# Kernel tuning notes

Measured on AMD Instinct MI355X. Metric: run time of the kernel, lower is better.

## Reference

```python
import jax, jax.numpy as jnp
import numpy as np

J, L, A, A_PRIME, C_CH = 4, 4, 2, 2, 1
B, M, N = 4, 128, 128


def _compute_idx():
    # mirrors CorrLayerDownsample.compute_idx with delta_j=J, delta_l=L,
    # shift_mode='samec' and num_channels=1 (to_shift_color always True)
    dj, dl = J, L
    la1, la2, shifted = [], [], []
    for c1 in range(C_CH):
        for c2 in range(C_CH):
            for j1 in range(J):
                for j2 in range(j1, min(j1 + 1 + dj, J)):
                    for l1 in range(L):
                        for l2 in range(max(0, l1 + 1 - dl), min(L, l1 + 1 + dl)):
                            for a1 in range(A):
                                for a2 in range(A_PRIME):
                                    la1.append((j1, A * L * c1 + A * l1 + a1))
                                    la2.append((j2, A * L * c2 + A * l2 + a2))
                                    shifted.append(j2 + 1)
    return (np.asarray(la1, np.int32), np.asarray(la2, np.int32),
            np.asarray(shifted, np.int32))


def _make_masks():
    # stand-in for create_masks_shift: mask 0 = zero shift only; mask k (k>=1)
    # = wrapped square neighborhood of radius 2**(k-1) (shift scale grows with j2)
    xs = np.minimum(np.arange(M), M - np.arange(M))
    ys = np.minimum(np.arange(N), N - np.arange(N))
    masks = np.zeros((J + 1, M, N), np.float32)
    masks[0, 0, 0] = 1.0
    for k in range(1, J + 1):
        r = 2 ** (k - 1)
        masks[k] = ((xs[:, None] <= r) & (ys[None, :] <= r)).astype(np.float32)
    return masks


def setup_inputs() -> dict:
    key = jax.random.key(0)
    la1, la2, shifted = _compute_idx()
    masks = _make_masks()
    union_idx = np.where(masks.sum(0).reshape(-1) > 0)[0].astype(np.int32)
    xpsi = jax.random.normal(key, (J, B, C_CH * L * A, M, N), dtype=jnp.float32)
    return {
        "xpsi": xpsi,
        "masks_shift": jnp.asarray(masks),
        "la1": jnp.asarray(la1),
        "la2": jnp.asarray(la2),
        "shifted": jnp.asarray(shifted),
        "union_idx": jnp.asarray(union_idx),
    }


def reference(xpsi, masks_shift, la1, la2, shifted, union_idx):
    # xpsi: [J, B, C, M, N] real. FFT once per (scale, channel) map.
    hatx = jnp.fft.fft2(xpsi)                     # [J, B, C, M, N] complex64
    # gather the (scale, la-channel) pair for every moment (all scales same size,
    # so the per-(j1,j2) loop + upsample of the original collapses to one gather)
    h1 = hatx[la1[:, 0], :, la1[:, 1]]            # [P, B, M, N]
    h2 = hatx[la2[:, 0], :, la2[:, 1]]            # [P, B, M, N]
    corr = jnp.fft.ifft2(h1 * jnp.conj(h2)).real  # [P, B, M, N]
    masked = corr * masks_shift[shifted][:, None]  # per-moment shift mask
    P, Bb, Mm, Nn = masked.shape
    # flatten=True path: keep only positions in the union of all shift masks
    return masked.reshape(P, Bb, Mm * Nn)[:, :, union_idx]
```

## Files before the change

### kernel.cpp

```cpp
#include <hip/hip_runtime.h>

typedef __attribute__((ext_vector_type(8))) short short8;
typedef __attribute__((ext_vector_type(4))) float float4v;
typedef __attribute__((address_space(1))) const unsigned int gu32;
typedef __attribute__((address_space(3))) unsigned int lu32;

#define TPB 256
#define NXPSI (4*4*8*16384)
#define NGR   (NXPSI/4)
#define ZPG   64
#define PBYTE (NXPSI*2 + ZPG*8)
#define NPART 3207168
#define NOUT  739840

__device__ __constant__ int TBASE[19] = {
    0, 278528, 557056, 835584, 1114112, 1392640, 1671168, 1949696, 2228224,
    2506752, 2617344, 2727936, 2838528, 2949120,
    3059712, 3100672, 3141632,
    3182592, 3194880};

static __device__ __forceinline__ unsigned short f2bf(float f) {
    unsigned int u = __builtin_bit_cast(unsigned int, f);
    u = (u + 0x7FFFu + ((u >> 16) & 1u)) >> 16;
    return (unsigned short)u;
}

__global__ __launch_bounds__(256)
void conv_bf16(const float* __restrict__ in, unsigned short* __restrict__ outw) {
    const int g = blockIdx.x * 256 + threadIdx.x;
    if (g < NGR) {
        const float4 v = reinterpret_cast<const float4*>(in)[g];
        reinterpret_cast<ushort4*>(outw)[g] =
            ushort4{f2bf(v.x), f2bf(v.y), f2bf(v.z), f2bf(v.w)};
    } else if (g < NGR + ZPG) {
        reinterpret_cast<ushort4*>(outw)[g] = ushort4{0, 0, 0, 0};
    }
}

template<int J2, bool PRE, bool PART>
static __device__ __forceinline__ void corr_body(
        const float* __restrict__ xpsi, const unsigned short* __restrict__ xbf,
        float* __restrict__ out, float* __restrict__ part,
        unsigned char* smem, int tgl, int n0, int moff, int b, int kc)
{
    constexpr int R    = 1 << J2;
    constexpr int DXN  = 2 * R + 1;
    constexpr int DYN  = DXN;
    constexpr int MV   = 8 * (J2 + 1);
    constexpr int ROWS = 16 + 2 * R;
    constexpr int ABUF = 16 * 256;
    constexpr int S    = DYN * MV * 16;
    constexpr int W    = (J2 == 0) ? 8 : 16;

    unsigned short* a_lds = (unsigned short*)smem;
    unsigned short* b_lds = (unsigned short*)(smem + 4 * ABUF);

    const int k0    = kc * 16;
    const int vrows = (MV - moff < 16) ? MV - moff : 16;

    const int ch2lo = n0 / DXN;
    int nhi = n0 + W - 1; if (nhi > 8 * DXN - 1) nhi = 8 * DXN - 1;
    const int nimg = nhi / DXN - ch2lo + 1;

    const int tid  = threadIdx.x;
    const int lane = tid & 63;
    const int wv   = tid >> 6;
    const int c    = lane & 15;
    const int g    = lane >> 4;

    const int ncol    = n0 + c;
    const bool validn = (ncol < 8 * DXN) && (J2 > 0 || c < 8);
    const int ncc     = validn ? ncol : n0;
    const int ch2     = ncc / DXN;
    const int dxi     = ncc - ch2 * DXN;
    const int dx      = dxi - R;
    const int xo      = dx < 0 ? dx + 17 : dx;
    const int bst     = ((ch2 - ch2lo) * ROWS + (2 * R - dxi)) * 152;

    auto stageA = [&](int sub, int bufi) {
        unsigned short* ab = a_lds + bufi * ABUF;
        #pragma unroll
        for (int it = 0; it < 2; ++it) {
            const int o  = it * TPB + tid;
            const int ms = o >> 5;
            const int lo = (o & 31) ^ ms;
            const int me = moff + ms;
            const int j1 = me >> 3, ch1 = me & 7;
            if (PRE) {
                const unsigned short* src = (ms < vrows)
                    ? xbf + ((((size_t)j1*4 + b)*8) + ch1) * 16384
                          + (k0 + sub * 2 + (lo >> 4)) * 128 + ((lo & 15) << 3)
                    : xbf + NXPSI + ((lo & 31) << 3);
                __builtin_amdgcn_global_load_lds((gu32*)src, (lu32*)(ab + o * 8), 16, 0, 0);
            } else {
                ushort4 w0{0,0,0,0}, w1{0,0,0,0};
                if (ms < vrows) {
                    const float* s = xpsi + ((((size_t)j1*4 + b)*8) + ch1) * 16384
                                   + (k0 + sub * 2 + (lo >> 4)) * 128 + ((lo & 15) << 3);
                    const float4 f0 = ((const float4*)s)[0];
                    const float4 f1 = ((const float4*)s)[1];
                    w0 = ushort4{f2bf(f0.x), f2bf(f0.y), f2bf(f0.z), f2bf(f0.w)};
                    w1 = ushort4{f2bf(f1.x), f2bf(f1.y), f2bf(f1.z), f2bf(f1.w)};
                }
                *(ushort4*)(ab + o * 8)     = w0;
                *(ushort4*)(ab + o * 8 + 4) = w1;
            }
        }
    };

    stageA(0, 0);

    if (PRE && J2 >= 2) {
        for (int ci = 0; ci < nimg; ++ci) {
            const unsigned short* img = xbf + ((((size_t)J2*4 + b)*8) + ch2lo + ci) * 16384;
            const int ng2 = ROWS * 36;
            for (int i = tid; i < ng2; i += TPB) {
                const int tr = i / 36, tc = (i - tr * 36) * 4;
                const int sr = (k0 - R + tr) & 127;
                const int sc = (tc + R - 16) & 127;
                *(ushort4*)(b_lds + (ci * ROWS + tr) * 152 + tc) =
                    *(const ushort4*)(img + sr * 128 + sc);
            }
        }
    } else {
        const int tot = nimg * ROWS * 144;
        for (int i = tid; i < tot; i += TPB) {
            const int ci = i / (ROWS * 144);
            const int rr = i - ci * (ROWS * 144);
            const int tr = rr / 144, tc = rr - tr * 144;
            const int sr = (k0 - R + tr) & 127;
            const int sc = (tc + R - 16) & 127;
            b_lds[(ci * ROWS + tr) * 152 + tc] = PRE
                ? xbf[((((size_t)J2*4 + b)*8) + ch2lo + ci) * 16384 + sr * 128 + sc]
                : f2bf(xpsi[((((size_t)J2*4 + b)*8) + ch2lo + ci) * 16384 + sr * 128 + sc]);
        }
    }

    float4v acc[DYN];
    #pragma unroll
    for (int i = 0; i < DYN; ++i) acc[i] = (float4v)0.f;

    auto compute = [&](int sub, int bufi) {
        const char* abase = (const char*)(a_lds + bufi * ABUF);
        #pragma unroll
        for (int i2 = 0; i2 < 2; ++i2) {
            const int loff = (((i2 << 8) | (wv << 6) | (g << 4))) ^ (c << 4);
            const short8 af0 = *(const short8*)(abase + c * 512 + loff);

            const unsigned short* bp = b_lds + bst + (sub * 2 + i2) * 152
                                     + (wv << 5) + (g << 3);
            const uint4 wA = *(const uint4*)bp;
            const uint4 wB = *(const uint4*)(bp + 8);
            const uint4 wC = *(const uint4*)(bp + 16);
            const unsigned int wd[12] = {wA.x,wA.y,wA.z,wA.w, wB.x,wB.y,wB.z,wB.w,
                                         wC.x,wC.y,wC.z,wC.w};
            __builtin_amdgcn_s_setprio(1);
            #pragma unroll
            for (int dyi = 0; dyi < DYN; ++dyi) {
                unsigned int o0, o1, o2, o3;
                if ((dyi & 1) == 0) {
                    const int bb = 8 - (dyi >> 1);
                    o0 = wd[bb]; o1 = wd[bb+1]; o2 = wd[bb+2]; o3 = wd[bb+3];
                } else {
                    const int bb = (15 - dyi) >> 1;
                    o0 = (wd[bb]   >> 16) | (wd[bb+1] << 16);
                    o1 = (wd[bb+1] >> 16) | (wd[bb+2] << 16);
                    o2 = (wd[bb+2] >> 16) | (wd[bb+3] << 16);
                    o3 = (wd[bb+3] >> 16) | (wd[bb+4] << 16);
                }
                union { unsigned int u[4]; short8 s; } bq;
                bq.u[0] = o0; bq.u[1] = o1; bq.u[2] = o2; bq.u[3] = o3;
                acc[dyi] = __builtin_amdgcn_mfma_f32_16x16x32_bf16(
                    af0, bq.s, acc[dyi], 0, 0, 0);
            }
            __builtin_amdgcn_s_setprio(0);
        }
    };

    __syncthreads();
    for (int sub = 0; sub < 8; ++sub) {
        if (sub < 7) stageA(sub + 1, (sub + 1) & 1);
        compute(sub, sub & 1);
        __syncthreads();
    }

    if (PART) {
        constexpr int NG  = (DYN < 9) ? DYN : 9;
        constexpr int NPH = (DYN + NG - 1) / NG;
        float* red = (float*)smem;
        float* pt  = part + TBASE[tgl] + (size_t)(kc * 4 + b) * S;
        const int cpart0 = n0 & 15;
        #pragma unroll
        for (int ph = 0; ph < NPH; ++ph) {
            const int d0 = ph * NG;
            const int nd = (DYN - d0 < NG) ? (DYN - d0) : NG;
            __syncthreads();
            #pragma unroll
            for (int dl = 0; dl < NG; ++dl) {
                if (dl >= nd) break;
                *(float4v*)(red + ((wv * NG + dl) * 64 + lane) * 4) = acc[d0 + dl];
            }
            __syncthreads();
            for (int i = tid; i < nd * 64; i += TPB) {
                const int dl = i >> 6;
                const int ln = i & 63;
                const float4v s0 = *(const float4v*)(red + ((0 * NG + dl) * 64 + ln) * 4);
                const float4v s1 = *(const float4v*)(red + ((1 * NG + dl) * 64 + ln) * 4);
                const float4v s2 = *(const float4v*)(red + ((2 * NG + dl) * 64 + ln) * 4);
                const float4v s3 = *(const float4v*)(red + ((3 * NG + dl) * 64 + ln) * 4);
                const float4v s = (s0 + s1) + (s2 + s3);
                const int cc = ln & 15, gg = ln >> 4;
                if ((n0 + cc < 8 * DXN) && (J2 > 0 || cc < 8)) {
                    const int dyi = d0 + dl;
                    #pragma unroll
                    for (int t2 = 0; t2 < 4; ++t2) {
                        const int ml = (gg << 2) + t2;
                        if (ml < vrows)
                            pt[(dyi * MV + moff + ml) * 16 + cpart0 + cc] = s[t2];
                    }
                }
            }
        }
        return;
    }

    if (!validn) return;
    #pragma unroll
    for (int dyi = 0; dyi < DYN; ++dyi) {
        const int dy = dyi - R;
        const int yo = dy < 0 ? dy + 17 : dy;
        #pragma unroll
        for (int t2 = 0; t2 < 4; ++t2) {
            const int ml = (g << 2) + t2;
            if (ml >= vrows) continue;
            const int m = moff + ml;
            const int j1 = m >> 3, ch1 = m & 7;
            const int pb = ((j1 * (9 - j1)) >> 1) + (J2 - j1);
            const int p  = pb * 64 + ((ch1 >> 1) << 4) + ((ch2 >> 1) << 2)
                         + ((ch1 & 1) << 1) + (ch2 & 1);
            atomicAdd(out + (size_t)(p * 4 + b) * 289 + xo * 17 + yo, acc[dyi][t2]);
        }
    }
}

template<bool PRE, bool PART>
__global__ __launch_bounds__(TPB, 3)
void corr_v8(const float* __restrict__ xpsi, const unsigned short* __restrict__ xbf,
             float* __restrict__ out, float* __restrict__ part)
{
    __shared__ __align__(16) unsigned char smem[40704];
    const int bid = blockIdx.x;
    const int g8  = bid & 7;
    const int b   = g8 >> 1;
    const int mh  = g8 & 1;
    const int w   = bid >> 3;
    const int kc  = w / 17;
    const int s   = w - kc * 17;
    if (s < 9)
        corr_body<3, PRE, PART>(xpsi, xbf, out, part, smem, s, 16 * s, 16 * mh, b, kc);
    else if (s < 14)
        corr_body<2, PRE, PART>(xpsi, xbf, out, part, smem, s, 16 * (s - 9), 16 * mh, b, kc);
    else if (mh == 0)
        corr_body<1, PRE, PART>(xpsi, xbf, out, part, smem, s, 16 * (s - 14), 0, b, kc);
    else
        corr_body<0, PRE, PART>(xpsi, xbf, out, part, smem,
                                (s < 16) ? 17 : 18, 8 * (s - 14), 0, b, kc);
}

__global__ __launch_bounds__(256)
void reduce2(const float* __restrict__ part, float* __restrict__ out)
{
    const int t  = blockIdx.y;
    const int j2 = (t < 9) ? 3 : (t < 14) ? 2 : (t < 17) ? 1 : 0;
    const int nt = t - ((t < 9) ? 0 : (t < 14) ? 9 : (t < 17) ? 14 : 17);
    const int R = 1 << j2, DXN = 2 * R + 1, DYN = DXN, MV = 8 * (j2 + 1);
    const int S = DYN * MV * 16;
    const int tot = 4 * DYN * MV * 4;
    const int i = blockIdx.x * 256 + threadIdx.x;
    if (i >= tot) return;
    const int c4 = (i & 3) << 2;
    int r2 = i >> 2;
    const int m = r2 % MV;  r2 /= MV;
    const int dyi = r2 % DYN;
    const int b   = r2 / DYN;
    const int ncol0 = nt * 16 + c4;
    if (ncol0 >= 8 * DXN) return;
    const float* q = part + TBASE[t] + (size_t)b * S + (dyi * MV + m) * 16 + c4;
    float4 v = {0.f, 0.f, 0.f, 0.f};
    #pragma unroll
    for (int qq = 0; qq < 8; ++qq) {
        const float4 w = *(const float4*)(q + (size_t)qq * 4 * S);
        v.x += w.x; v.y += w.y; v.z += w.z; v.w += w.w;
    }
    const int dy = dyi - R;
    const int yo = dy < 0 ? dy + 17 : dy;
    const int j1 = m >> 3, ch1 = m & 7;
    const int pb = ((j1 * (9 - j1)) >> 1) + (j2 - j1);
    const float vv[4] = {v.x, v.y, v.z, v.w};
    #pragma unroll
    for (int e = 0; e < 4; ++e) {
        const int ncol = ncol0 + e;
        if (ncol >= 8 * DXN) break;
        const int ch2 = ncol / DXN;
        const int dxi = ncol - ch2 * DXN;
        const int dx  = dxi - R;
        const int xo  = dx < 0 ? dx + 17 : dx;
        const int p   = pb * 64 + ((ch1 >> 1) << 4) + ((ch2 >> 1) << 2)
                      + ((ch1 & 1) << 1) + (ch2 & 1);
        out[(size_t)(p * 4 + b) * 289 + xo * 17 + yo] = vv[e];
    }
}

extern "C" void kernel_launch(void* const* d_in, const int* in_sizes, int n_in,
                              void* d_out, int out_size, void* d_ws, size_t ws_size,
                              hipStream_t stream) {
    const float* xpsi = (const float*)d_in[0];
    float* out = (float*)d_out;

    if (ws_size >= (size_t)PBYTE + (size_t)NPART * 4) {
        unsigned short* xbf = (unsigned short*)d_ws;
        float* part = (float*)((char*)d_ws + PBYTE);
        hipMemsetAsync(d_out, 0, (size_t)out_size * sizeof(float), stream);
        conv_bf16<<<(NGR + ZPG + 255) / 256, 256, 0, stream>>>(xpsi, xbf);
        corr_v8<true, true><<<1088, TPB, 0, stream>>>(xpsi, xbf, out, part);
        reduce2<<<dim3(34, 19), 256, 0, stream>>>(part, out);
    } else if (ws_size >= (size_t)PBYTE) {
        unsigned short* xbf = (unsigned short*)d_ws;
        hipMemsetAsync(d_out, 0, (size_t)out_size * sizeof(float), stream);
        conv_bf16<<<(NGR + ZPG + 255) / 256, 256, 0, stream>>>(xpsi, xbf);
        corr_v8<true, false><<<1088, TPB, 0, stream>>>(xpsi, xbf, out, nullptr);
    } else {
        hipMemsetAsync(d_out, 0, (size_t)out_size * sizeof(float), stream);
        corr_v8<false, false><<<1088, TPB, 0, stream>>>(xpsi, nullptr, out, nullptr);
    }
}
```

Measured before the change: 46.23 us.

## Fuse bf16 conversion into correlation kernel and write every output in reduce

Drops the separate fp32-to-bf16 pre-pass and the bf16 workspace copy. The correlation kernel now loads fp32 tiles into registers, converts them, and writes them to LDS after the MFMA compute step, so the global loads overlap with compute. The reduce kernel is rewritten to cover every output element, writing zeros outside the shift masks, which removes the output memset. This saves two launches and one full pass over the input, at the cost of twice the global read bytes in the main kernel and more registers held across compute; the s_setprio hints are also removed.

After: 45.35 us. Within noise of the previous version (-1.9%).

```diff
diff --git a/kernel.cpp b/kernel.cpp
--- a/kernel.cpp
+++ b/kernel.cpp
@@ -2,14 +2,8 @@
 
 typedef __attribute__((ext_vector_type(8))) short short8;
 typedef __attribute__((ext_vector_type(4))) float float4v;
-typedef __attribute__((address_space(1))) const unsigned int gu32;
-typedef __attribute__((address_space(3))) unsigned int lu32;
 
 #define TPB 256
-#define NXPSI (4*4*8*16384)
-#define NGR   (NXPSI/4)
-#define ZPG   64
-#define PBYTE (NXPSI*2 + ZPG*8)
 #define NPART 3207168
 #define NOUT  739840
 
@@ -18,6 +12,9 @@
     2506752, 2617344, 2727936, 2838528, 2949120,
     3059712, 3100672, 3141632,
     3182592, 3194880};
+__device__ __constant__ unsigned char J1T[10] = {0,0,0,0,1,1,1,2,2,3};
+__device__ __constant__ unsigned char J2T[10] = {0,1,2,3,1,2,3,2,3,3};
+__device__ __constant__ unsigned char TSTART[4] = {17,14,9,0};
 
 static __device__ __forceinline__ unsigned short f2bf(float f) {
     unsigned int u = __builtin_bit_cast(unsigned int, f);
@@ -25,21 +22,9 @@
     return (unsigned short)u;
 }
 
-__global__ __launch_bounds__(256)
-void conv_bf16(const float* __restrict__ in, unsigned short* __restrict__ outw) {
-    const int g = blockIdx.x * 256 + threadIdx.x;
-    if (g < NGR) {
-        const float4 v = reinterpret_cast<const float4*>(in)[g];
-        reinterpret_cast<ushort4*>(outw)[g] =
-            ushort4{f2bf(v.x), f2bf(v.y), f2bf(v.z), f2bf(v.w)};
-    } else if (g < NGR + ZPG) {
-        reinterpret_cast<ushort4*>(outw)[g] = ushort4{0, 0, 0, 0};
-    }
-}
-
-template<int J2, bool PRE, bool PART>
+template<int J2, bool PART>
 static __device__ __forceinline__ void corr_body(
-        const float* __restrict__ xpsi, const unsigned short* __restrict__ xbf,
+        const float* __restrict__ xpsi,
         float* __restrict__ out, float* __restrict__ part,
         unsigned char* smem, int tgl, int n0, int moff, int b, int kc)
 {
@@ -77,8 +62,8 @@
     const int xo      = dx < 0 ? dx + 17 : dx;
     const int bst     = ((ch2 - ch2lo) * ROWS + (2 * R - dxi)) * 152;
 
-    auto stageA = [&](int sub, int bufi) {
-        unsigned short* ab = a_lds + bufi * ABUF;
+    float4 ar[4];
+    auto loadA = [&](int sub) {
         #pragma unroll
         for (int it = 0; it < 2; ++it) {
             const int o  = it * TPB + tid;
@@ -86,40 +71,41 @@
             const int lo = (o & 31) ^ ms;
             const int me = moff + ms;
             const int j1 = me >> 3, ch1 = me & 7;
-            if (PRE) {
-                const unsigned short* src = (ms < vrows)
-                    ? xbf + ((((size_t)j1*4 + b)*8) + ch1) * 16384
-                          + (k0 + sub * 2 + (lo >> 4)) * 128 + ((lo & 15) << 3)
-                    : xbf + NXPSI + ((lo & 31) << 3);
-                __builtin_amdgcn_global_load_lds((gu32*)src, (lu32*)(ab + o * 8), 16, 0, 0);
+            if (ms < vrows) {
+                const float* s = xpsi + ((((size_t)j1*4 + b)*8) + ch1) * 16384
+                               + (k0 + sub * 2 + (lo >> 4)) * 128 + ((lo & 15) << 3);
+                ar[2*it]   = ((const float4*)s)[0];
+                ar[2*it+1] = ((const float4*)s)[1];
             } else {
-                ushort4 w0{0,0,0,0}, w1{0,0,0,0};
-                if (ms < vrows) {
-                    const float* s = xpsi + ((((size_t)j1*4 + b)*8) + ch1) * 16384
-                                   + (k0 + sub * 2 + (lo >> 4)) * 128 + ((lo & 15) << 3);
-                    const float4 f0 = ((const float4*)s)[0];
-                    const float4 f1 = ((const float4*)s)[1];
-                    w0 = ushort4{f2bf(f0.x), f2bf(f0.y), f2bf(f0.z), f2bf(f0.w)};
-                    w1 = ushort4{f2bf(f1.x), f2bf(f1.y), f2bf(f1.z), f2bf(f1.w)};
-                }
-                *(ushort4*)(ab + o * 8)     = w0;
-                *(ushort4*)(ab + o * 8 + 4) = w1;
+                ar[2*it]   = float4{0.f,0.f,0.f,0.f};
+                ar[2*it+1] = float4{0.f,0.f,0.f,0.f};
             }
         }
     };
-
-    stageA(0, 0);
-
-    if (PRE && J2 >= 2) {
+    auto writeA = [&](int bufi) {
+        unsigned short* ab = a_lds + bufi * ABUF;
+        #pragma unroll
+        for (int it = 0; it < 2; ++it) {
+            const int o = it * TPB + tid;
+            const float4 f0 = ar[2*it], f1 = ar[2*it+1];
+            *(ushort4*)(ab + o * 8)     = ushort4{f2bf(f0.x),f2bf(f0.y),f2bf(f0.z),f2bf(f0.w)};
+            *(ushort4*)(ab + o * 8 + 4) = ushort4{f2bf(f1.x),f2bf(f1.y),f2bf(f1.z),f2bf(f1.w)};
+        }
+    };
+
+    loadA(0);
+
+    if (J2 >= 2) {
         for (int ci = 0; ci < nimg; ++ci) {
-            const unsigned short* img = xbf + ((((size_t)J2*4 + b)*8) + ch2lo + ci) * 16384;
+            const float* img = xpsi + ((((size_t)J2*4 + b)*8) + ch2lo + ci) * 16384;
             const int ng2 = ROWS * 36;
             for (int i = tid; i < ng2; i += TPB) {
                 const int tr = i / 36, tc = (i - tr * 36) * 4;
                 const int sr = (k0 - R + tr) & 127;
                 const int sc = (tc + R - 16) & 127;
+                const float4 v = *(const float4*)(img + sr * 128 + sc);
                 *(ushort4*)(b_lds + (ci * ROWS + tr) * 152 + tc) =
-                    *(const ushort4*)(img + sr * 128 + sc);
+                    ushort4{f2bf(v.x), f2bf(v.y), f2bf(v.z), f2bf(v.w)};
             }
         }
     } else {
@@ -130,11 +116,12 @@
             const int tr = rr / 144, tc = rr - tr * 144;
             const int sr = (k0 - R + tr) & 127;
             const int sc = (tc + R - 16) & 127;
-            b_lds[(ci * ROWS + tr) * 152 + tc] = PRE
-                ? xbf[((((size_t)J2*4 + b)*8) + ch2lo + ci) * 16384 + sr * 128 + sc]
-                : f2bf(xpsi[((((size_t)J2*4 + b)*8) + ch2lo + ci) * 16384 + sr * 128 + sc]);
-        }
-    }
+            b_lds[(ci * ROWS + tr) * 152 + tc] =
+                f2bf(xpsi[((((size_t)J2*4 + b)*8) + ch2lo + ci) * 16384 + sr * 128 + sc]);
+        }
+    }
+
+    writeA(0);
 
     float4v acc[DYN];
     #pragma unroll
@@ -154,7 +141,6 @@
             const uint4 wC = *(const uint4*)(bp + 16);
             const unsigned int wd[12] = {wA.x,wA.y,wA.z,wA.w, wB.x,wB.y,wB.z,wB.w,
                                          wC.x,wC.y,wC.z,wC.w};
-            __builtin_amdgcn_s_setprio(1);
             #pragma unroll
             for (int dyi = 0; dyi < DYN; ++dyi) {
                 unsigned int o0, o1, o2, o3;
@@ -173,14 +159,14 @@
                 acc[dyi] = __builtin_amdgcn_mfma_f32_16x16x32_bf16(
                     af0, bq.s, acc[dyi], 0, 0, 0);
             }
-            __builtin_amdgcn_s_setprio(0);
         }
     };
 
     __syncthreads();
     for (int sub = 0; sub < 8; ++sub) {
-        if (sub < 7) stageA(sub + 1, (sub + 1) & 1);
+        if (sub < 7) loadA(sub + 1);
         compute(sub, sub & 1);
+        if (sub < 7) writeA((sub + 1) & 1);
         __syncthreads();
     }
 
@@ -243,9 +229,9 @@
     }
 }
 
-template<bool PRE, bool PART>
+template<bool PART>
 __global__ __launch_bounds__(TPB, 3)
-void corr_v8(const float* __restrict__ xpsi, const unsigned short* __restrict__ xbf,
+void corr_v9(const float* __restrict__ xpsi,
              float* __restrict__ out, float* __restrict__ part)
 {
     __shared__ __align__(16) unsigned char smem[40704];
@@ -257,58 +243,47 @@
     const int kc  = w / 17;
     const int s   = w - kc * 17;
     if (s < 9)
-        corr_body<3, PRE, PART>(xpsi, xbf, out, part, smem, s, 16 * s, 16 * mh, b, kc);
+        corr_body<3, PART>(xpsi, out, part, smem, s, 16 * s, 16 * mh, b, kc);
     else if (s < 14)
-        corr_body<2, PRE, PART>(xpsi, xbf, out, part, smem, s, 16 * (s - 9), 16 * mh, b, kc);
+        corr_body<2, PART>(xpsi, out, part, smem, s, 16 * (s - 9), 16 * mh, b, kc);
     else if (mh == 0)
-        corr_body<1, PRE, PART>(xpsi, xbf, out, part, smem, s, 16 * (s - 14), 0, b, kc);
+        corr_body<1, PART>(xpsi, out, part, smem, s, 16 * (s - 14), 0, b, kc);
     else
-        corr_body<0, PRE, PART>(xpsi, xbf, out, part, smem,
-                                (s < 16) ? 17 : 18, 8 * (s - 14), 0, b, kc);
+        corr_body<0, PART>(xpsi, out, part, smem,
+                           (s < 16) ? 17 : 18, 8 * (s - 14), 0, b, kc);
 }
 
 __global__ __launch_bounds__(256)
-void reduce2(const float* __restrict__ part, float* __restrict__ out)
+void reduce_k(const float* __restrict__ part, float* __restrict__ out)
 {
-    const int t  = blockIdx.y;
-    const int j2 = (t < 9) ? 3 : (t < 14) ? 2 : (t < 17) ? 1 : 0;
-    const int nt = t - ((t < 9) ? 0 : (t < 14) ? 9 : (t < 17) ? 14 : 17);
-    const int R = 1 << j2, DXN = 2 * R + 1, DYN = DXN, MV = 8 * (j2 + 1);
-    const int S = DYN * MV * 16;
-    const int tot = 4 * DYN * MV * 4;
-    const int i = blockIdx.x * 256 + threadIdx.x;
-    if (i >= tot) return;
-    const int c4 = (i & 3) << 2;
-    int r2 = i >> 2;
-    const int m = r2 % MV;  r2 /= MV;
-    const int dyi = r2 % DYN;
-    const int b   = r2 / DYN;
-    const int ncol0 = nt * 16 + c4;
-    if (ncol0 >= 8 * DXN) return;
-    const float* q = part + TBASE[t] + (size_t)b * S + (dyi * MV + m) * 16 + c4;
-    float4 v = {0.f, 0.f, 0.f, 0.f};
-    #pragma unroll
-    for (int qq = 0; qq < 8; ++qq) {
-        const float4 w = *(const float4*)(q + (size_t)qq * 4 * S);
-        v.x += w.x; v.y += w.y; v.z += w.z; v.w += w.w;
-    }
-    const int dy = dyi - R;
-    const int yo = dy < 0 ? dy + 17 : dy;
-    const int j1 = m >> 3, ch1 = m & 7;
-    const int pb = ((j1 * (9 - j1)) >> 1) + (j2 - j1);
-    const float vv[4] = {v.x, v.y, v.z, v.w};
-    #pragma unroll
-    for (int e = 0; e < 4; ++e) {
-        const int ncol = ncol0 + e;
-        if (ncol >= 8 * DXN) break;
-        const int ch2 = ncol / DXN;
-        const int dxi = ncol - ch2 * DXN;
-        const int dx  = dxi - R;
-        const int xo  = dx < 0 ? dx + 17 : dx;
-        const int p   = pb * 64 + ((ch1 >> 1) << 4) + ((ch2 >> 1) << 2)
-                      + ((ch1 & 1) << 1) + (ch2 & 1);
-        out[(size_t)(p * 4 + b) * 289 + xo * 17 + yo] = vv[e];
-    }
+    const int o = blockIdx.x * 256 + threadIdx.x;
+    if (o >= NOUT) return;
+    const int p  = o / 1156;
+    const int r1 = o - p * 1156;
+    const int b  = r1 / 289;
+    const int s  = r1 - b * 289;
+    const int xo = s / 17, yo = s - xo * 17;
+    const int pb = p >> 6, cc = p & 63;
+    const int j1 = J1T[pb], j2 = J2T[pb];
+    const int R  = 1 << j2;
+    const int dx = xo <= 8 ? xo : xo - 17;
+    const int dy = yo <= 8 ? yo : yo - 17;
+    float v = 0.f;
+    if (dx >= -R && dx <= R && dy >= -R && dy <= R) {
+        const int ch1 = ((cc >> 4) & 3) * 2 + ((cc >> 1) & 1);
+        const int ch2 = ((cc >> 2) & 3) * 2 + (cc & 1);
+        const int DYN = 2 * R + 1, MV = 8 * (j2 + 1);
+        const int ncol = ch2 * DYN + (dx + R);
+        const int t = TSTART[j2] + (ncol >> 4);
+        const int c = ncol & 15;
+        const int m = j1 * 8 + ch1;
+        const int S = DYN * MV * 16;
+        const float* q = part + TBASE[t]
+                       + ((size_t)(b * DYN + (dy + R)) * MV + m) * 16 + c;
+        #pragma unroll
+        for (int kc = 0; kc < 8; ++kc) v += q[(size_t)kc * 4 * S];
+    }
+    out[o] = v;
 }
 
 extern "C" void kernel_launch(void* const* d_in, const int* in_sizes, int n_in,
@@ -317,20 +292,12 @@
     const float* xpsi = (const float*)d_in[0];
     float* out = (float*)d_out;
 
-    if (ws_size >= (size_t)PBYTE + (size_t)NPART * 4) {
-        unsigned short* xbf = (unsigned short*)d_ws;
-        float* part = (float*)((char*)d_ws + PBYTE);
-        hipMemsetAsync(d_out, 0, (size_t)out_size * sizeof(float), stream);
-        conv_bf16<<<(NGR + ZPG + 255) / 256, 256, 0, stream>>>(xpsi, xbf);
-        corr_v8<true, true><<<1088, TPB, 0, stream>>>(xpsi, xbf, out, part);
-        reduce2<<<dim3(34, 19), 256, 0, stream>>>(part, out);
-    } else if (ws_size >= (size_t)PBYTE) {
-        unsigned short* xbf = (unsigned short*)d_ws;
-        hipMemsetAsync(d_out, 0, (size_t)out_size * sizeof(float), stream);
-        conv_bf16<<<(NGR + ZPG + 255) / 256, 256, 0, stream>>>(xpsi, xbf);
-        corr_v8<true, false><<<1088, TPB, 0, stream>>>(xpsi, xbf, out, nullptr);
+    if (ws_size >= (size_t)NPART * 4) {
+        float* part = (float*)d_ws;
+        corr_v9<true><<<1088, TPB, 0, stream>>>(xpsi, out, part);
+        reduce_k<<<(NOUT + 255) / 256, 256, 0, stream>>>(part, out);
     } else {
         hipMemsetAsync(d_out, 0, (size_t)out_size * sizeof(float), stream);
-        corr_v8<false, false><<<1088, TPB, 0, stream>>>(xpsi, nullptr, out, nullptr);
-    }
-}
+        corr_v9<false><<<1088, TPB, 0, stream>>>(xpsi, out, nullptr);
+    }
+}
```
